# Performance work log

Hardware: AMD Instinct MI355X
Metric: run time of the kernel (lower is better)

## Reference

```python
import jax, jax.numpy as jnp
import numpy as np

L = 128          # bandlimit (max_l)
NTHETA = 256     # Gauss-Legendre latitudes (>= L for exact quadrature)
NPHI = 512       # longitudes (>= 2L-1)
C_IN, C_OUT = 32, 32


def _normalized_assoc_legendre(Lmax, xg):
    """Pbar_lm(x) with Condon-Shortley phase, orthonormal on the sphere.
    Returns (Lmax, Lmax, T) for m>=0; zero for m>l."""
    T = xg.shape[0]
    P = np.zeros((Lmax, Lmax, T), dtype=np.float64)
    sx = np.sqrt(np.maximum(1.0 - xg * xg, 0.0))
    P[0, 0] = 1.0 / np.sqrt(4.0 * np.pi)
    for m in range(1, Lmax):
        P[m, m] = -np.sqrt((2 * m + 1) / (2.0 * m)) * sx * P[m - 1, m - 1]
    for m in range(0, Lmax - 1):
        P[m + 1, m] = np.sqrt(2 * m + 3.0) * xg * P[m, m]
    for m in range(Lmax):
        for l in range(m + 2, Lmax):
            a = np.sqrt((4.0 * l * l - 1.0) / (l * l - m * m))
            b = np.sqrt(((l - 1.0) ** 2 - m * m) / (4.0 * (l - 1.0) ** 2 - 1.0))
            P[l, m] = a * (xg * P[l - 1, m] - b * P[l - 2, m])
    return P


def _build_basis():
    # Gauss-Legendre quadrature in cos(theta): exact for degree <= 2*NTHETA-1
    xg, wg = np.polynomial.legendre.leggauss(NTHETA)
    P = _normalized_assoc_legendre(L, xg)  # (L, L, T), m>=0
    # Full basis B[l, m+L-1, t]; Pbar_{l,-m} = (-1)^m Pbar_{l,m}
    B = np.zeros((L, 2 * L - 1, NTHETA), dtype=np.float64)
    for m in range(-(L - 1), L):
        B[:, m + L - 1, :] = ((-1.0) ** abs(m) if m < 0 else 1.0) * P[:, abs(m), :]
    return B.astype(np.float32), wg.astype(np.float32)


def setup_inputs() -> dict:
    key = jax.random.key(0)
    k1, k2, k3 = jax.random.split(key, 3)
    x = jax.random.normal(k1, (NTHETA, NPHI, C_IN), dtype=jnp.float32)
    std = 1.0 / (C_IN + C_OUT)
    wr = std * jax.random.normal(k2, (L, 2 * L - 1, C_IN, C_OUT), dtype=jnp.float32)
    wi = std * jax.random.normal(k3, (L, 2 * L - 1, C_IN, C_OUT), dtype=jnp.float32)
    B, wg = _build_basis()
    return {"x": x, "weights_real": wr, "weights_imag": wi,
            "legendre": jnp.asarray(B), "quad_w": jnp.asarray(wg)}


def reference(x, weights_real, weights_imag, legendre, quad_w):
    ntheta, nphi, _ = x.shape
    Lb = legendre.shape[0]
    # --- forward SHT (per channel, vectorized) ---
    # longitude FFT: Fm[t,k,c] = sum_p x e^{-i 2pi k p / nphi}; dphi = 2pi/nphi
    Fm = jnp.fft.fft(x.astype(jnp.complex64), axis=1) * (2.0 * np.pi / nphi)
    midx = np.arange(-(Lb - 1), Lb) % nphi            # FFT bins for m=-(L-1)..L-1
    Fm_sel = Fm[:, midx, :]                           # (t, 2L-1, c)
    Bw = legendre * quad_w[None, None, :]             # quadrature-weighted basis
    # flm[l,m,c] = sum_t w_t Pbar_lm(theta_t) Fm[t,m,c]
    flm = jnp.einsum('lmt,tmc->lmc', Bw.astype(jnp.complex64), Fm_sel)
    # --- spectral conv: per-(l,m) channel mixing ---
    W = weights_real.astype(jnp.complex64) + 1j * weights_imag.astype(jnp.complex64)
    y = jnp.einsum('lmc,lmco->lmo', flm, W)           # (L, 2L-1, O)
    # --- inverse SHT ---
    G = jnp.einsum('lmt,lmo->tmo', legendre.astype(jnp.complex64), y)  # (t, 2L-1, O)
    spec = jnp.zeros((ntheta, nphi, G.shape[-1]), dtype=jnp.complex64)
    spec = spec.at[:, midx, :].set(G)
    out = jnp.fft.ifft(spec, axis=1) * nphi           # f = sum_m G e^{i m phi}
    return jnp.moveaxis(out.real, 2, 0)               # (O, ntheta, nphi)
```

## Files before the change

### kernel.cpp

```cpp
#include <hip/hip_runtime.h>
#include <math.h>

#define DEVFN __global__ __launch_bounds__(256)

namespace {
constexpr int LL  = 128;
constexpr int MM2 = 255;
constexpr int NT  = 256;
constexpr int NP  = 512;
constexpr int NC  = 32;
constexpr int NO  = 32;
constexpr float TWO_PI = 6.283185307179586476925286766559f;
}

typedef short v8s __attribute__((ext_vector_type(8)));
typedef float v4f __attribute__((ext_vector_type(4)));

__device__ inline unsigned short f2bf(float f) {
  unsigned int u = __float_as_uint(f);
  return (unsigned short)((u + 0x7FFFu + ((u >> 16) & 1u)) >> 16);
}

DEVFN void k0_twiddle(unsigned short* __restrict__ tw1t, unsigned short* __restrict__ vt) {
  const int idx = blockIdx.x * 256 + threadIdx.x;
  const float phi = TWO_PI / (float)NP;
  const float fs  = TWO_PI / (float)NP;
  {
    const int n = idx >> 9, p = idx & 511;
    const int m = n >> 1;
    const int k = (m * p) & (NP - 1);
    float s, c;
    sincosf(phi * (float)k, &s, &c);
    tw1t[idx] = f2bf((n & 1) ? (-s * fs) : (c * fs));
  }
  {
    const int p = idx >> 8, k = idx & 255;
    const int m = k >> 1;
    const int kk = (m * p) & (NP - 1);
    float s, c;
    sincosf(phi * (float)kk, &s, &c);
    vt[idx] = f2bf((k & 1) ? s : c);
  }
}

DEVFN void k0b_xpose(const float* __restrict__ x, unsigned short* __restrict__ xb) {
  __shared__ float sm[32][65];
  const int t = blockIdx.x;
  const int p0 = blockIdx.y * 64;
  const int tid = threadIdx.x;
#pragma unroll
  for (int i = 0; i < 8; ++i) {
    const int idx = tid + i * 256;
    const int p = idx >> 5, c = idx & 31;
    sm[c][p] = x[((size_t)t * NP + p0 + p) * NC + c];
  }
  __syncthreads();
  const int c = tid >> 3, pg = tid & 7;
  unsigned short pk[8];
#pragma unroll
  for (int u = 0; u < 8; ++u) pk[u] = f2bf(sm[c][pg * 8 + u]);
  *(uint4*)(xb + ((size_t)(t * 32 + c)) * NP + p0 + pg * 8) = *(const uint4*)pk;
}

DEVFN void k1_mfma(const unsigned short* __restrict__ xb,
                   const unsigned short* __restrict__ tw1t,
                   const float* __restrict__ wg,
                   float* __restrict__ fwr, float* __restrict__ fwi) {
  __shared__ unsigned short As[128 * 32];
  __shared__ unsigned short Bs[128 * 32];
  const int tid = threadIdx.x;
  const int r0 = blockIdx.x * 128;
  const int n0 = blockIdx.y * 128;
  const int wid = tid >> 6, lane = tid & 63;
  const int wm = wid & 1, wn = wid >> 1;
  v4f acc[4][4];
#pragma unroll
  for (int i = 0; i < 4; ++i)
#pragma unroll
    for (int j = 0; j < 4; ++j) {
      acc[i][j][0] = 0.f; acc[i][j][1] = 0.f; acc[i][j][2] = 0.f; acc[i][j][3] = 0.f;
    }
  const int lr = lane & 15, lk = (lane >> 4) * 8;
  for (int k0 = 0; k0 < 512; k0 += 32) {
#pragma unroll
    for (int s = 0; s < 2; ++s) {
      const int chunk = tid + s * 256;
      const int row = chunk >> 2, c16 = chunk & 3;
      *(uint4*)&As[row * 32 + c16 * 8] =
          *(const uint4*)&xb[(size_t)(r0 + row) * 512 + k0 + c16 * 8];
      *(uint4*)&Bs[row * 32 + c16 * 8] =
          *(const uint4*)&tw1t[(size_t)(n0 + row) * 512 + k0 + c16 * 8];
    }
    __syncthreads();
    v8s af[4], bf[4];
#pragma unroll
    for (int i = 0; i < 4; ++i) af[i] = *(const v8s*)&As[(wm * 64 + i * 16 + lr) * 32 + lk];
#pragma unroll
    for (int j = 0; j < 4; ++j) bf[j] = *(const v8s*)&Bs[(wn * 64 + j * 16 + lr) * 32 + lk];
#pragma unroll
    for (int i = 0; i < 4; ++i)
#pragma unroll
      for (int j = 0; j < 4; ++j)
        acc[i][j] = __builtin_amdgcn_mfma_f32_16x16x32_bf16(af[i], bf[j], acc[i][j], 0, 0, 0);
    __syncthreads();
  }
  const int lrow = (lane >> 4) * 4;
#pragma unroll
  for (int i = 0; i < 4; ++i) {
    const int rbase = r0 + wm * 64 + i * 16 + lrow;
#pragma unroll
    for (int j = 0; j < 4; ++j) {
      const int n = n0 + wn * 64 + j * 16 + lr;
      const int mI = n >> 1;
      float* dst = (n & 1) ? fwi : fwr;
#pragma unroll
      for (int reg = 0; reg < 4; ++reg) {
        const int r = rbase + reg;
        const int t = r >> 5, c = r & 31;
        dst[((size_t)mI * NT + t) * NC + c] = acc[i][j][reg] * wg[t];
      }
    }
  }
}

DEVFN void k2_flm(const float* __restrict__ leg, const float* __restrict__ fwr,
                  const float* __restrict__ fwi, float* __restrict__ flr,
                  float* __restrict__ fli) {
  const int m = blockIdx.x;
  const int l = m + blockIdx.y * 8 + (threadIdx.x >> 5);
  const int c = threadIdx.x & 31;
  if (l >= LL) return;
  const float* lg = leg + ((size_t)(l * MM2 + 127 + m)) * NT;
  const float* fr = fwr + (size_t)m * NT * NC + c;
  const float* fi = fwi + (size_t)m * NT * NC + c;
  float ar = 0.f, ai = 0.f;
  for (int t = 0; t < NT; t += 4) {
#pragma unroll
    for (int u = 0; u < 4; ++u) {
      const float b = lg[t + u];
      ar = fmaf(b, fr[(t + u) * NC], ar);
      ai = fmaf(b, fi[(t + u) * NC], ai);
    }
  }
  flr[(m * LL + l) * NC + c] = ar;
  fli[(m * LL + l) * NC + c] = ai;
}

DEVFN void k3_y(const float* __restrict__ wr, const float* __restrict__ wi,
                const float* __restrict__ flr, const float* __restrict__ fli,
                float* __restrict__ ya, float* __restrict__ yb) {
  const int m = blockIdx.x;
  const int lbase = m + (int)blockIdx.y * 32;
  if (lbase >= LL) return;
  __shared__ float sfr[32][33];
  __shared__ float sfi[32][33];
  const int tid = threadIdx.x;
  for (int i = tid; i < 1024; i += 256) {
    const int lr2 = i >> 5, cc = i & 31;
    const int l = lbase + lr2;
    sfr[lr2][cc] = (l < LL) ? flr[(m * LL + l) * NC + cc] : 0.f;
    sfi[lr2][cc] = (l < LL) ? fli[(m * LL + l) * NC + cc] : 0.f;
  }
  __syncthreads();
  const int lo = tid >> 3;
  const int o4 = (tid & 7) << 2;
  const int l = lbase + lo;
  if (l >= LL) return;
  const float s0 = (m > 0) ? 1.0f : 0.0f;
  const size_t base_p = ((size_t)(l * MM2 + 127 + m) * NC) * NO + o4;
  const size_t base_n = ((size_t)(l * MM2 + 127 - m) * NC) * NO + o4;
  float ax = 0, ay = 0, az = 0, aw = 0;
  float bx = 0, by = 0, bz = 0, bw = 0;
#pragma unroll 4
  for (int c = 0; c < NC; ++c) {
    const float fr = sfr[lo][c], fi = sfi[lo][c];
    const float4 pr = *(const float4*)(wr + base_p + c * NO);
    const float4 nr = *(const float4*)(wr + base_n + c * NO);
    const float4 pi = *(const float4*)(wi + base_p + c * NO);
    const float4 ni = *(const float4*)(wi + base_n + c * NO);
    const float wax = pr.x + s0 * nr.x, way = pr.y + s0 * nr.y,
                waz = pr.z + s0 * nr.z, waw = pr.w + s0 * nr.w;
    const float wbx = s0 * ni.x - pi.x, wby = s0 * ni.y - pi.y,
                wbz = s0 * ni.z - pi.z, wbw = s0 * ni.w - pi.w;
    ax = fmaf(fr, wax, fmaf(fi, wbx, ax));
    ay = fmaf(fr, way, fmaf(fi, wby, ay));
    az = fmaf(fr, waz, fmaf(fi, wbz, az));
    aw = fmaf(fr, waw, fmaf(fi, wbw, aw));
    bx = fmaf(fr, wbx, fmaf(-fi, wax, bx));
    by = fmaf(fr, wby, fmaf(-fi, way, by));
    bz = fmaf(fr, wbz, fmaf(-fi, waz, bz));
    bw = fmaf(fr, wbw, fmaf(-fi, waw, bw));
  }
  float4 va = {ax, ay, az, aw}, vb = {bx, by, bz, bw};
  *(float4*)(ya + (size_t)(m * LL + l) * NO + o4) = va;
  *(float4*)(yb + (size_t)(m * LL + l) * NO + o4) = vb;
}

DEVFN void k4_G(const float* __restrict__ leg, const float* __restrict__ ya,
                const float* __restrict__ yb, unsigned short* __restrict__ ut) {
  const int m = blockIdx.x;
  const int o = threadIdx.x & 31;
  const int tq = threadIdx.x >> 5;
  const int t0 = blockIdx.y * 32 + tq * 4;
  float aa[4] = {}, bb[4] = {};
  for (int l = m; l < LL; ++l) {
    const float* lgl = leg + ((size_t)(l * MM2 + 127 + m)) * NT + t0;
    const float yav = ya[(m * LL + l) * NO + o];
    const float ybv = yb[(m * LL + l) * NO + o];
#pragma unroll
    for (int i = 0; i < 4; ++i) {
      const float g = lgl[i];
      aa[i] = fmaf(g, yav, aa[i]);
      bb[i] = fmaf(g, ybv, bb[i]);
    }
  }
#pragma unroll
  for (int i = 0; i < 4; ++i) {
    const unsigned int pk = (unsigned int)f2bf(aa[i]) | ((unsigned int)f2bf(bb[i]) << 16);
    *(unsigned int*)&ut[((size_t)((t0 + i) * 32 + o)) * 256 + 2 * m] = pk;
  }
}

DEVFN void k5_mfma(const unsigned short* __restrict__ ut,
                   const unsigned short* __restrict__ vt,
                   float* __restrict__ out) {
  __shared__ unsigned short As[128 * 32];
  __shared__ unsigned short Bs[128 * 32];
  const int tid = threadIdx.x;
  const int r0 = blockIdx.x * 128;
  const int p0 = blockIdx.y * 128;
  const int wid = tid >> 6, lane = tid & 63;
  const int wm = wid & 1, wn = wid >> 1;
  v4f acc[4][4];
#pragma unroll
  for (int i = 0; i < 4; ++i)
#pragma unroll
    for (int j = 0; j < 4; ++j) {
      acc[i][j][0] = 0.f; acc[i][j][1] = 0.f; acc[i][j][2] = 0.f; acc[i][j][3] = 0.f;
    }
  const int lr = lane & 15, lk = (lane >> 4) * 8;
  for (int k0 = 0; k0 < 256; k0 += 32) {
#pragma unroll
    for (int s = 0; s < 2; ++s) {
      const int chunk = tid + s * 256;
      const int row = chunk >> 2, c16 = chunk & 3;
      *(uint4*)&As[row * 32 + c16 * 8] =
          *(const uint4*)&ut[(size_t)(r0 + row) * 256 + k0 + c16 * 8];
      *(uint4*)&Bs[row * 32 + c16 * 8] =
          *(const uint4*)&vt[(size_t)(p0 + row) * 256 + k0 + c16 * 8];
    }
    __syncthreads();
    v8s af[4], bf[4];
#pragma unroll
    for (int i = 0; i < 4; ++i) af[i] = *(const v8s*)&As[(wm * 64 + i * 16 + lr) * 32 + lk];
#pragma unroll
    for (int j = 0; j < 4; ++j) bf[j] = *(const v8s*)&Bs[(wn * 64 + j * 16 + lr) * 32 + lk];
#pragma unroll
    for (int i = 0; i < 4; ++i)
#pragma unroll
      for (int j = 0; j < 4; ++j)
        acc[i][j] = __builtin_amdgcn_mfma_f32_16x16x32_bf16(af[i], bf[j], acc[i][j], 0, 0, 0);
    __syncthreads();
  }
  const int lrow = (lane >> 4) * 4;
#pragma unroll
  for (int i = 0; i < 4; ++i) {
    const int rbase = r0 + wm * 64 + i * 16 + lrow;
#pragma unroll
    for (int j = 0; j < 4; ++j) {
      const int p = p0 + wn * 64 + j * 16 + lr;
#pragma unroll
      for (int reg = 0; reg < 4; ++reg) {
        const int r = rbase + reg;
        const int t = r >> 5, o = r & 31;
        out[((size_t)o * NT + t) * NP + p] = acc[i][j][reg];
      }
    }
  }
}

extern "C" void kernel_launch(void* const* d_in, const int* in_sizes, int n_in,
                              void* d_out, int out_size, void* d_ws, size_t ws_size,
                              hipStream_t stream) {
  const float* x   = (const float*)d_in[0];
  const float* wr  = (const float*)d_in[1];
  const float* wi  = (const float*)d_in[2];
  const float* leg = (const float*)d_in[3];
  const float* wg  = (const float*)d_in[4];
  float* out = (float*)d_out;

  unsigned short* tw1t = (unsigned short*)d_ws;
  unsigned short* vt   = tw1t + 131072;
  unsigned short* xb   = vt + 131072;
  unsigned short* ut   = xb + 4194304;
  float* fwr = (float*)(ut + 2097152);
  float* fwi = fwr + 1048576;
  float* flr = fwi + 1048576;
  float* fli = flr + 524288;
  float* ya  = fli + 524288;
  float* yb  = ya + 524288;

  hipLaunchKernelGGL(k0_twiddle, dim3(512), dim3(256), 0, stream, tw1t, vt);
  hipLaunchKernelGGL(k0b_xpose, dim3(256, 8), dim3(256), 0, stream, x, xb);
  hipLaunchKernelGGL(k1_mfma, dim3(64, 2), dim3(256), 0, stream, xb, tw1t, wg, fwr, fwi);
  hipLaunchKernelGGL(k2_flm, dim3(128, 16), dim3(256), 0, stream, leg, fwr, fwi, flr, fli);
  hipLaunchKernelGGL(k3_y, dim3(128, 4), dim3(256), 0, stream, wr, wi, flr, fli, ya, yb);
  hipLaunchKernelGGL(k4_G, dim3(128, 8), dim3(256), 0, stream, leg, ya, yb, ut);
  hipLaunchKernelGGL(k5_mfma, dim3(64, 4), dim3(256), 0, stream, ut, vt, out);
}
```

Measured before the change: 405.6 us.

## Merge prep kernels and vectorize MFMA epilogue stores via operand swap

The twiddle-generation and input-transpose kernels are merged into one launch with a block-index split, removing one kernel launch. The k1 epilogue now writes four consecutive channels per lane as a float4 with a single quadrature weight per row group. In k5 the A/B operands are swapped so the accumulator's four registers run along the longitude axis, which allows float4 stores to the output instead of scattered scalar writes. The k5 grid is transposed to match. This targets uncoalesced global stores and launch overhead, at the cost of a divergent branch in the merged prep kernel.

```diff
diff --git a/kernel.cpp b/kernel.cpp
--- a/kernel.cpp
+++ b/kernel.cpp
@@ -21,45 +21,48 @@
   return (unsigned short)((u + 0x7FFFu + ((u >> 16) & 1u)) >> 16);
 }
 
-DEVFN void k0_twiddle(unsigned short* __restrict__ tw1t, unsigned short* __restrict__ vt) {
-  const int idx = blockIdx.x * 256 + threadIdx.x;
+DEVFN void kp_prep(const float* __restrict__ x, unsigned short* __restrict__ tw1t,
+                   unsigned short* __restrict__ vt, unsigned short* __restrict__ xb) {
+  __shared__ float sm[32][65];
+  const int bid = blockIdx.x;
+  const int tid = threadIdx.x;
   const float phi = TWO_PI / (float)NP;
-  const float fs  = TWO_PI / (float)NP;
-  {
-    const int n = idx >> 9, p = idx & 511;
-    const int m = n >> 1;
-    const int k = (m * p) & (NP - 1);
-    float s, c;
-    sincosf(phi * (float)k, &s, &c);
-    tw1t[idx] = f2bf((n & 1) ? (-s * fs) : (c * fs));
-  }
-  {
-    const int p = idx >> 8, k = idx & 255;
-    const int m = k >> 1;
-    const int kk = (m * p) & (NP - 1);
-    float s, c;
-    sincosf(phi * (float)kk, &s, &c);
-    vt[idx] = f2bf((k & 1) ? s : c);
-  }
-}
-
-DEVFN void k0b_xpose(const float* __restrict__ x, unsigned short* __restrict__ xb) {
-  __shared__ float sm[32][65];
-  const int t = blockIdx.x;
-  const int p0 = blockIdx.y * 64;
-  const int tid = threadIdx.x;
-#pragma unroll
-  for (int i = 0; i < 8; ++i) {
-    const int idx = tid + i * 256;
-    const int p = idx >> 5, c = idx & 31;
-    sm[c][p] = x[((size_t)t * NP + p0 + p) * NC + c];
-  }
-  __syncthreads();
-  const int c = tid >> 3, pg = tid & 7;
-  unsigned short pk[8];
-#pragma unroll
-  for (int u = 0; u < 8; ++u) pk[u] = f2bf(sm[c][pg * 8 + u]);
-  *(uint4*)(xb + ((size_t)(t * 32 + c)) * NP + p0 + pg * 8) = *(const uint4*)pk;
+  if (bid < 512) {
+    const int idx = bid * 256 + tid;
+    const float fs = TWO_PI / (float)NP;
+    {
+      const int n = idx >> 9, p = idx & 511;
+      const int m = n >> 1;
+      const int k = (m * p) & (NP - 1);
+      float s, c;
+      sincosf(phi * (float)k, &s, &c);
+      tw1t[idx] = f2bf((n & 1) ? (-s * fs) : (c * fs));
+    }
+    {
+      const int p = idx >> 8, k = idx & 255;
+      const int m = k >> 1;
+      const int kk = (m * p) & (NP - 1);
+      float s, c;
+      sincosf(phi * (float)kk, &s, &c);
+      vt[idx] = f2bf((k & 1) ? s : c);
+    }
+  } else {
+    const int q = bid - 512;
+    const int t = q >> 3;
+    const int p0 = (q & 7) * 64;
+#pragma unroll
+    for (int i = 0; i < 8; ++i) {
+      const int idx = tid + i * 256;
+      const int p = idx >> 5, c = idx & 31;
+      sm[c][p] = x[((size_t)t * NP + p0 + p) * NC + c];
+    }
+    __syncthreads();
+    const int c = tid >> 3, pg = tid & 7;
+    unsigned short pk[8];
+#pragma unroll
+    for (int u = 0; u < 8; ++u) pk[u] = f2bf(sm[c][pg * 8 + u]);
+    *(uint4*)(xb + ((size_t)(t * 32 + c)) * NP + p0 + pg * 8) = *(const uint4*)pk;
+  }
 }
 
 DEVFN void k1_mfma(const unsigned short* __restrict__ xb,
@@ -108,17 +111,15 @@
 #pragma unroll
   for (int i = 0; i < 4; ++i) {
     const int rbase = r0 + wm * 64 + i * 16 + lrow;
+    const int t = rbase >> 5, c0 = rbase & 31;
+    const float w = wg[t];
 #pragma unroll
     for (int j = 0; j < 4; ++j) {
       const int n = n0 + wn * 64 + j * 16 + lr;
       const int mI = n >> 1;
       float* dst = (n & 1) ? fwi : fwr;
-#pragma unroll
-      for (int reg = 0; reg < 4; ++reg) {
-        const int r = rbase + reg;
-        const int t = r >> 5, c = r & 31;
-        dst[((size_t)mI * NT + t) * NC + c] = acc[i][j][reg] * wg[t];
-      }
+      float4 v = {acc[i][j][0] * w, acc[i][j][1] * w, acc[i][j][2] * w, acc[i][j][3] * w};
+      *(float4*)&dst[((size_t)mI * NT + t) * NC + c0] = v;
     }
   }
 }
@@ -227,8 +228,8 @@
   __shared__ unsigned short As[128 * 32];
   __shared__ unsigned short Bs[128 * 32];
   const int tid = threadIdx.x;
-  const int r0 = blockIdx.x * 128;
-  const int p0 = blockIdx.y * 128;
+  const int p0 = blockIdx.x * 128;
+  const int r0 = blockIdx.y * 128;
   const int wid = tid >> 6, lane = tid & 63;
   const int wm = wid & 1, wn = wid >> 1;
   v4f acc[4][4];
@@ -245,9 +246,9 @@
       const int chunk = tid + s * 256;
       const int row = chunk >> 2, c16 = chunk & 3;
       *(uint4*)&As[row * 32 + c16 * 8] =
+          *(const uint4*)&vt[(size_t)(p0 + row) * 256 + k0 + c16 * 8];
+      *(uint4*)&Bs[row * 32 + c16 * 8] =
           *(const uint4*)&ut[(size_t)(r0 + row) * 256 + k0 + c16 * 8];
-      *(uint4*)&Bs[row * 32 + c16 * 8] =
-          *(const uint4*)&vt[(size_t)(p0 + row) * 256 + k0 + c16 * 8];
     }
     __syncthreads();
     v8s af[4], bf[4];
@@ -265,16 +266,13 @@
   const int lrow = (lane >> 4) * 4;
 #pragma unroll
   for (int i = 0; i < 4; ++i) {
-    const int rbase = r0 + wm * 64 + i * 16 + lrow;
+    const int pbase = p0 + wm * 64 + i * 16 + lrow;
 #pragma unroll
     for (int j = 0; j < 4; ++j) {
-      const int p = p0 + wn * 64 + j * 16 + lr;
-#pragma unroll
-      for (int reg = 0; reg < 4; ++reg) {
-        const int r = rbase + reg;
-        const int t = r >> 5, o = r & 31;
-        out[((size_t)o * NT + t) * NP + p] = acc[i][j][reg];
-      }
+      const int r = r0 + wn * 64 + j * 16 + lr;
+      const int t = r >> 5, o = r & 31;
+      float4 v = {acc[i][j][0], acc[i][j][1], acc[i][j][2], acc[i][j][3]};
+      *(float4*)&out[((size_t)o * NT + t) * NP + pbase] = v;
     }
   }
 }
@@ -300,11 +298,10 @@
   float* ya  = fli + 524288;
   float* yb  = ya + 524288;
 
-  hipLaunchKernelGGL(k0_twiddle, dim3(512), dim3(256), 0, stream, tw1t, vt);
-  hipLaunchKernelGGL(k0b_xpose, dim3(256, 8), dim3(256), 0, stream, x, xb);
+  hipLaunchKernelGGL(kp_prep, dim3(2560), dim3(256), 0, stream, x, tw1t, vt, xb);
   hipLaunchKernelGGL(k1_mfma, dim3(64, 2), dim3(256), 0, stream, xb, tw1t, wg, fwr, fwi);
   hipLaunchKernelGGL(k2_flm, dim3(128, 16), dim3(256), 0, stream, leg, fwr, fwi, flr, fli);
   hipLaunchKernelGGL(k3_y, dim3(128, 4), dim3(256), 0, stream, wr, wi, flr, fli, ya, yb);
   hipLaunchKernelGGL(k4_G, dim3(128, 8), dim3(256), 0, stream, leg, ya, yb, ut);
-  hipLaunchKernelGGL(k5_mfma, dim3(64, 4), dim3(256), 0, stream, ut, vt, out);
-}
+  hipLaunchKernelGGL(k5_mfma, dim3(4, 64), dim3(256), 0, stream, ut, vt, out);
+}
```

Result: no change. 412.8 us (+1.8%).
